# Kernel tuning notes

Measured on AMD Instinct MI355X. Metric: run time of the kernel, lower is better.

## Reference

```python
import jax, jax.numpy as jnp
import numpy as np

B, L, J, D_MODEL, N_HIDDEN = 8, 2048, 2048, 1024, 1024


def setup_inputs() -> dict:
    key = jax.random.key(0)
    ks = jax.random.split(key, 6)
    scale = 1.0 / np.sqrt(D_MODEL)
    return {
        "q": jax.random.normal(ks[0], (B, L, D_MODEL), dtype=jnp.float32),
        "k": jax.random.normal(ks[1], (B, J, D_MODEL), dtype=jnp.float32),
        "v": jax.random.normal(ks[2], (B, J, D_MODEL), dtype=jnp.float32),
        "mask": jnp.zeros((B, L, J), dtype=jnp.float32),
        # Linear(d_model, n_hidden, bias=False) weights, stored [n_hidden, d_model] like torch
        "W_q": jax.random.normal(ks[3], (N_HIDDEN, D_MODEL), dtype=jnp.float32) * scale,
        "W_k": jax.random.normal(ks[4], (N_HIDDEN, D_MODEL), dtype=jnp.float32) * scale,
        "W_v": jax.random.normal(ks[5], (N_HIDDEN, D_MODEL), dtype=jnp.float32) * scale,
    }


def reference(q, k, v, mask, W_q, W_k, W_v):
    # Linear projections (torch Linear: x @ W.T)
    qp = jnp.einsum('bld,hd->blh', q, W_q)
    kp = jnp.einsum('bjd,hd->bjh', k, W_k)
    vp = jnp.einsum('bjd,hd->bjh', v, W_v)
    # scaled dot-product scores [B, L, J]
    scores = jnp.einsum('blh,bjh->blj', qp, kp) / jnp.sqrt(jnp.float32(N_HIDDEN)).astype(qp.dtype)
    scores = scores + mask
    attn = jax.nn.softmax(scores, axis=-1)
    return jnp.einsum('blj,bjh->blh', attn, vp)
```

## Files before the change

kernel.cpp:

```cpp
#include <hip/hip_runtime.h>
#include <hip/hip_fp16.h>

typedef _Float16 f16;
typedef __attribute__((ext_vector_type(8))) _Float16 f16x8;
typedef __attribute__((ext_vector_type(4))) _Float16 f16x4;
typedef __attribute__((ext_vector_type(4))) float f32x4;

#define BM 256
#define BN 256
#define BK 32

__device__ __forceinline__ void gll16(const void* src, void* dst) {
  __builtin_amdgcn_global_load_lds((const __attribute__((address_space(1))) void*)src,
                                   (__attribute__((address_space(3))) void*)dst,
                                   16, 0, 0);
}

template<int MODE>
__global__ __launch_bounds__(512, 2)
void gemm_bt(const f16* __restrict__ Aall, const f16* __restrict__ Ball,
             void* __restrict__ Call,
             int M, int N, int K, int lda, int ldb, int ldc,
             long strideA, long strideB, long strideC,
             const float* __restrict__ maskAll, long strideMask,
             float* __restrict__ lvec, float scale)
{
  __shared__ __align__(16) f16 smA[3][BM * BK];
  __shared__ __align__(16) f16 smB[3][BN * BK];

  unsigned gx = gridDim.x, gy = gridDim.y;
  unsigned id = (blockIdx.z * gy + blockIdx.y) * gx + blockIdx.x;
  unsigned nwg = gx * gy * gridDim.z;
  unsigned swz = (id & 7) * (nwg >> 3) + (id >> 3);
  unsigned bx = swz % gx, rem = swz / gx;
  unsigned by = rem % gy, bz = rem / gy;

  const int z = bz;
  const f16* A = Aall + (long)z * strideA;
  const f16* B = Ball + (long)z * strideB;

  const int tid  = threadIdx.x;
  const int wid  = tid >> 6;
  const int lane = tid & 63;
  const int wm = wid >> 2;
  const int wn = wid & 3;
  const int lr = lane & 15;
  const int g  = lane >> 4;

  const long brow = (long)by * BM;
  const long bcol = (long)bx * BN;
  const int  nt   = K / BK;

  f32x4 acc[8][4] = {};

  auto stA = [&](int buf, int t) {
    #pragma unroll
    for (int i = 0; i < 2; ++i) {
      int c   = i * 512 + tid;
      int row = c >> 2;
      gll16(A + (brow + row) * (long)lda + t * BK + (c & 3) * 8, &smA[buf][c * 8]);
    }
  };
  auto stB = [&](int buf, int t) {
    #pragma unroll
    for (int i = 0; i < 2; ++i) {
      int c   = i * 512 + tid;
      int row = c >> 2;
      gll16(B + (bcol + row) * (long)ldb + t * BK + (c & 3) * 8, &smB[buf][c * 8]);
    }
  };
  auto ld = [&](const f16* base, int r) -> f16x8 {
    return *(const f16x8*)(base + r * BK + g * 8);
  };

  stA(0, 0); stB(0, 0);
  stA(1, 1); stB(1, 1);
  asm volatile("s_waitcnt vmcnt(4)" ::: "memory");
  __builtin_amdgcn_s_barrier();

  int b0 = 0, bn = 2;
  for (int kt = 0; kt < nt; ++kt) {
    const f16* sa = smA[b0];
    const f16* sb = smB[b0];
    const bool pf = (kt + 2 < nt);
    f16x8 af[4], bf[4];

    #pragma unroll
    for (int n = 0; n < 4; ++n) bf[n] = ld(sb, wn * 64 + n * 16 + lr);
    #pragma unroll
    for (int m = 0; m < 4; ++m) af[m] = ld(sa, wm * 128 + m * 16 + lr);
    if (pf) stA(bn, kt + 2);
    __builtin_amdgcn_s_barrier();
    asm volatile("s_waitcnt lgkmcnt(0)" ::: "memory");
    __builtin_amdgcn_sched_barrier(0);
    __builtin_amdgcn_s_setprio(1);
    #pragma unroll
    for (int m = 0; m < 4; ++m)
      #pragma unroll
      for (int n = 0; n < 4; ++n)
        acc[m][n] = __builtin_amdgcn_mfma_f32_16x16x32_f16(af[m], bf[n], acc[m][n], 0, 0, 0);
    __builtin_amdgcn_s_setprio(0);
    __builtin_amdgcn_s_barrier();

    #pragma unroll
    for (int m = 0; m < 4; ++m) af[m] = ld(sa, wm * 128 + 64 + m * 16 + lr);
    if (pf) stB(bn, kt + 2);
    __builtin_amdgcn_s_barrier();
    asm volatile("s_waitcnt lgkmcnt(0)" ::: "memory");
    __builtin_amdgcn_sched_barrier(0);
    __builtin_amdgcn_s_setprio(1);
    #pragma unroll
    for (int m = 0; m < 4; ++m)
      #pragma unroll
      for (int n = 0; n < 4; ++n)
        acc[m + 4][n] = __builtin_amdgcn_mfma_f32_16x16x32_f16(af[m], bf[n], acc[m + 4][n], 0, 0, 0);
    __builtin_amdgcn_s_setprio(0);
    __builtin_amdgcn_sched_barrier(0);
    if (pf) { asm volatile("s_waitcnt vmcnt(4)" ::: "memory"); }
    else    { asm volatile("s_waitcnt vmcnt(0)" ::: "memory"); }
    __builtin_amdgcn_s_barrier();
    b0 = b0 + 1 == 3 ? 0 : b0 + 1;
    bn = bn + 1 == 3 ? 0 : bn + 1;
  }

  const int rb = (lane >> 4) * 4;

  if (MODE == 0) {
    f16* C = (f16*)Call + (long)z * strideC;
    #pragma unroll
    for (int m = 0; m < 8; ++m)
      #pragma unroll
      for (int j = 0; j < 4; ++j) {
        long grow = brow + wm * 128 + m * 16 + rb + j;
        #pragma unroll
        for (int n = 0; n < 4; ++n) {
          long gcol = bcol + wn * 64 + n * 16 + lr;
          C[grow * ldc + gcol] = (f16)acc[m][n][j];
        }
      }
  } else if (MODE == 1) {
    f16* C = (f16*)Call + (long)z * strideC;
    const float* mask = maskAll + (long)z * strideMask;
    #pragma unroll
    for (int m = 0; m < 8; ++m)
      #pragma unroll
      for (int j = 0; j < 4; ++j) {
        long grow = brow + wm * 128 + m * 16 + rb + j;
        float s = 0.f;
        #pragma unroll
        for (int n = 0; n < 4; ++n) {
          long gcol = bcol + wn * 64 + n * 16 + lr;
          float p = __expf(acc[m][n][j] * scale + mask[grow * ldc + gcol]);
          C[grow * ldc + gcol] = (f16)p;
          s += p;
        }
        s += __shfl_xor(s, 1);
        s += __shfl_xor(s, 2);
        s += __shfl_xor(s, 4);
        s += __shfl_xor(s, 8);
        if (lr == 0)
          lvec[((long)z * M + grow) * 32 + bx * 4 + wn] = s;
      }
  } else {
    float* C = (float*)Call + (long)z * strideC;
    #pragma unroll
    for (int m = 0; m < 8; ++m)
      #pragma unroll
      for (int j = 0; j < 4; ++j) {
        long grow = brow + wm * 128 + m * 16 + rb + j;
        float inv = 1.0f / lvec[(long)z * M + grow];
        #pragma unroll
        for (int n = 0; n < 4; ++n) {
          long gcol = bcol + wn * 64 + n * 16 + lr;
          C[grow * ldc + gcol] = acc[m][n][j] * inv;
        }
      }
  }
}

__global__ void cvt_all(const float* __restrict__ q, const float* __restrict__ k,
                        const float* __restrict__ v, const float* __restrict__ Wq,
                        const float* __restrict__ Wk, const float* __restrict__ Wv,
                        f16* __restrict__ qf, f16* __restrict__ kf, f16* __restrict__ vf,
                        f16* __restrict__ Wqf, f16* __restrict__ Wkf, f16* __restrict__ Wvf)
{
  const long NQ4 = 4194304, NW4 = 262144;
  const long total = 3 * NQ4 + 3 * NW4;
  for (long i = (long)blockIdx.x * blockDim.x + threadIdx.x; i < total;
       i += (long)gridDim.x * blockDim.x) {
    const float* src; f16* dst; long j = i;
    if      (j <     NQ4)           { src = q;  dst = qf; }
    else if (j < 2 * NQ4)           { src = k;  dst = kf;  j -= NQ4; }
    else if (j < 3 * NQ4)           { src = v;  dst = vf;  j -= 2 * NQ4; }
    else if (j < 3 * NQ4 + NW4)     { src = Wq; dst = Wqf; j -= 3 * NQ4; }
    else if (j < 3 * NQ4 + 2 * NW4) { src = Wk; dst = Wkf; j -= 3 * NQ4 + NW4; }
    else                            { src = Wv; dst = Wvf; j -= 3 * NQ4 + 2 * NW4; }
    float4 vv = ((const float4*)src)[j];
    f16x4 o;
    o[0] = (f16)vv.x; o[1] = (f16)vv.y; o[2] = (f16)vv.z; o[3] = (f16)vv.w;
    ((f16x4*)dst)[j] = o;
  }
}

__global__ void reduce_l(const float* __restrict__ lpart, float* __restrict__ lsum, int n) {
  int i = blockIdx.x * blockDim.x + threadIdx.x;
  if (i < n) {
    float s = 0.f;
    #pragma unroll
    for (int j = 0; j < 32; ++j) s += lpart[(long)i * 32 + j];
    lsum[i] = s;
  }
}

extern "C" void kernel_launch(void* const* d_in, const int* in_sizes, int n_in,
                              void* d_out, int out_size, void* d_ws, size_t ws_size,
                              hipStream_t stream)
{
  const float* q    = (const float*)d_in[0];
  const float* k    = (const float*)d_in[1];
  const float* v    = (const float*)d_in[2];
  const float* mask = (const float*)d_in[3];
  const float* Wq   = (const float*)d_in[4];
  const float* Wk   = (const float*)d_in[5];
  const float* Wv   = (const float*)d_in[6];
  float* out = (float*)d_out;
  char*  ws  = (char*)d_ws;

  f16* qf  = (f16*)(ws + 0);
  f16* kf  = (f16*)(ws + 33554432);
  f16* vf  = (f16*)(ws + 67108864);
  f16* Pm  = (f16*)(ws + 0);
  f16* Wqf = (f16*)(ws + 100663296);
  f16* Wkf = (f16*)(ws + 102760448);
  f16* Wvf = (f16*)(ws + 104857600);
  f16* qp  = (f16*)(ws + 106954752);
  f16* kp  = (f16*)(ws + 140509184);
  f16* vpT = (f16*)(ws + 174063616);
  float* lpart = (float*)(ws + 207618048);
  float* lsum  = (float*)(ws + 209715200);

  const long L = 2048, J = 2048, D = 1024, H = 1024;

  cvt_all<<<dim3(2048), dim3(256), 0, stream>>>(q, k, v, Wq, Wk, Wv, qf, kf, vf, Wqf, Wkf, Wvf);

  gemm_bt<0><<<dim3(1024 / BN, 16384 / BM, 1), dim3(512), 0, stream>>>(
      qf, Wqf, qp, 16384, 1024, 1024, 1024, 1024, 1024,
      0, 0, 0, nullptr, 0, nullptr, 0.f);
  gemm_bt<0><<<dim3(1024 / BN, 16384 / BM, 1), dim3(512), 0, stream>>>(
      kf, Wkf, kp, 16384, 1024, 1024, 1024, 1024, 1024,
      0, 0, 0, nullptr, 0, nullptr, 0.f);
  gemm_bt<0><<<dim3(2048 / BN, 1024 / BM, 8), dim3(512), 0, stream>>>(
      Wvf, vf, vpT, 1024, 2048, 1024, 1024, 1024, 2048,
      0, J * D, H * J, nullptr, 0, nullptr, 0.f);

  gemm_bt<1><<<dim3(2048 / BN, 2048 / BM, 8), dim3(512), 0, stream>>>(
      qp, kp, Pm, 2048, 2048, 1024, 1024, 1024, 2048,
      L * H, J * H, L * J, mask, L * J, lpart, 0.03125f);

  reduce_l<<<dim3(16384 / 256), dim3(256), 0, stream>>>(lpart, lsum, 16384);

  gemm_bt<2><<<dim3(1024 / BN, 2048 / BM, 8), dim3(512), 0, stream>>>(
      Pm, vpT, out, 2048, 1024, 2048, 2048, 2048, 1024,
      L * J, H * J, L * H, nullptr, 0, lsum, 0.f);
}
```

Before: 385.3 us.

## Deepen GEMM K-tile to 64 with XOR-swizzled LDS and quarter-tile ping-pong pipeline

```diff
diff --git a/kernel.cpp b/kernel.cpp
--- a/kernel.cpp
+++ b/kernel.cpp
@@ -8,7 +8,7 @@
 
 #define BM 256
 #define BN 256
-#define BK 32
+#define BK 64
 
 __device__ __forceinline__ void gll16(const void* src, void* dst) {
   __builtin_amdgcn_global_load_lds((const __attribute__((address_space(1))) void*)src,
@@ -25,8 +25,8 @@
              const float* __restrict__ maskAll, long strideMask,
              float* __restrict__ lvec, float scale)
 {
-  __shared__ __align__(16) f16 smA[3][BM * BK];
-  __shared__ __align__(16) f16 smB[3][BN * BK];
+  __shared__ __align__(16) f16 smA[2][BM * BK];
+  __shared__ __align__(16) f16 smB[2][BN * BK];
 
   unsigned gx = gridDim.x, gy = gridDim.y;
   unsigned id = (blockIdx.z * gy + blockIdx.y) * gx + blockIdx.x;
@@ -52,75 +52,92 @@
   const int  nt   = K / BK;
 
   f32x4 acc[8][4] = {};
-
-  auto stA = [&](int buf, int t) {
+  f16x8 af[8], bf[8];
+
+  auto stage_half = [&](f16* dst, const f16* src, long prow, int ld_, int rowOff, int t) {
     #pragma unroll
     for (int i = 0; i < 2; ++i) {
-      int c   = i * 512 + tid;
-      int row = c >> 2;
-      gll16(A + (brow + row) * (long)lda + t * BK + (c & 3) * 8, &smA[buf][c * 8]);
+      int c  = i * 512 + tid;
+      int r  = c >> 3;
+      int sl = (c & 7) ^ (r & 7);
+      gll16(src + (prow + rowOff + r) * (long)ld_ + t * BK + sl * 8,
+            dst + rowOff * BK + c * 8);
     }
   };
-  auto stB = [&](int buf, int t) {
-    #pragma unroll
-    for (int i = 0; i < 2; ++i) {
-      int c   = i * 512 + tid;
-      int row = c >> 2;
-      gll16(B + (bcol + row) * (long)ldb + t * BK + (c & 3) * 8, &smB[buf][c * 8]);
-    }
-  };
-  auto ld = [&](const f16* base, int r) -> f16x8 {
-    return *(const f16x8*)(base + r * BK + g * 8);
-  };
-
-  stA(0, 0); stB(0, 0);
-  stA(1, 1); stB(1, 1);
-  asm volatile("s_waitcnt vmcnt(4)" ::: "memory");
-  __builtin_amdgcn_s_barrier();
-
-  int b0 = 0, bn = 2;
-  for (int kt = 0; kt < nt; ++kt) {
-    const f16* sa = smA[b0];
-    const f16* sb = smB[b0];
-    const bool pf = (kt + 2 < nt);
-    f16x8 af[4], bf[4];
-
-    #pragma unroll
-    for (int n = 0; n < 4; ++n) bf[n] = ld(sb, wn * 64 + n * 16 + lr);
-    #pragma unroll
-    for (int m = 0; m < 4; ++m) af[m] = ld(sa, wm * 128 + m * 16 + lr);
-    if (pf) stA(bn, kt + 2);
+  auto rdA = [&](const f16* sa, int mh) {
+    #pragma unroll
+    for (int fm = 0; fm < 4; ++fm)
+      #pragma unroll
+      for (int ks = 0; ks < 2; ++ks) {
+        int r = wm * 128 + mh * 64 + fm * 16 + lr;
+        af[fm * 2 + ks] = *(const f16x8*)(sa + r * BK + ((ks * 4 + g) ^ (r & 7)) * 8);
+      }
+  };
+  auto rdB = [&](const f16* sb, int nh) {
+    #pragma unroll
+    for (int fn = 0; fn < 2; ++fn)
+      #pragma unroll
+      for (int ks = 0; ks < 2; ++ks) {
+        int r = wn * 64 + (nh * 2 + fn) * 16 + lr;
+        bf[(nh * 2 + fn) * 2 + ks] = *(const f16x8*)(sb + r * BK + ((ks * 4 + g) ^ (r & 7)) * 8);
+      }
+  };
+  auto sync_mfma = [&](int fm0, int fn0) {
     __builtin_amdgcn_s_barrier();
     asm volatile("s_waitcnt lgkmcnt(0)" ::: "memory");
     __builtin_amdgcn_sched_barrier(0);
     __builtin_amdgcn_s_setprio(1);
     #pragma unroll
-    for (int m = 0; m < 4; ++m)
-      #pragma unroll
-      for (int n = 0; n < 4; ++n)
-        acc[m][n] = __builtin_amdgcn_mfma_f32_16x16x32_f16(af[m], bf[n], acc[m][n], 0, 0, 0);
+    for (int fm = 0; fm < 4; ++fm)
+      #pragma unroll
+      for (int fn = 0; fn < 2; ++fn)
+        #pragma unroll
+        for (int ks = 0; ks < 2; ++ks)
+          acc[fm0 + fm][fn0 + fn] = __builtin_amdgcn_mfma_f32_16x16x32_f16(
+              af[fm * 2 + ks], bf[(fn0 + fn) * 2 + ks], acc[fm0 + fm][fn0 + fn], 0, 0, 0);
     __builtin_amdgcn_s_setprio(0);
     __builtin_amdgcn_s_barrier();
-
-    #pragma unroll
-    for (int m = 0; m < 4; ++m) af[m] = ld(sa, wm * 128 + 64 + m * 16 + lr);
-    if (pf) stB(bn, kt + 2);
-    __builtin_amdgcn_s_barrier();
-    asm volatile("s_waitcnt lgkmcnt(0)" ::: "memory");
-    __builtin_amdgcn_sched_barrier(0);
-    __builtin_amdgcn_s_setprio(1);
-    #pragma unroll
-    for (int m = 0; m < 4; ++m)
-      #pragma unroll
-      for (int n = 0; n < 4; ++n)
-        acc[m + 4][n] = __builtin_amdgcn_mfma_f32_16x16x32_f16(af[m], bf[n], acc[m + 4][n], 0, 0, 0);
-    __builtin_amdgcn_s_setprio(0);
-    __builtin_amdgcn_sched_barrier(0);
-    if (pf) { asm volatile("s_waitcnt vmcnt(4)" ::: "memory"); }
-    else    { asm volatile("s_waitcnt vmcnt(0)" ::: "memory"); }
-    __builtin_amdgcn_s_barrier();
-    b0 = b0 + 1 == 3 ? 0 : b0 + 1;
-    bn = bn + 1 == 3 ? 0 : bn + 1;
+  };
+
+  stage_half(smA[0], A, brow, lda, 0, 0);
+  stage_half(smA[0], A, brow, lda, 128, 0);
+  stage_half(smB[0], B, bcol, ldb, 0, 0);
+  stage_half(smB[0], B, bcol, ldb, 128, 0);
+  stage_half(smB[1], B, bcol, ldb, 0, 1);
+  stage_half(smB[1], B, bcol, ldb, 128, 1);
+  asm volatile("s_waitcnt vmcnt(4)" ::: "memory");
+  __builtin_amdgcn_s_barrier();
+
+  const int niter = nt / 2;
+  for (int i = 0; i < niter; ++i) {
+    const bool last = (i == niter - 1);
+    const int t2 = 2 * i + 2, t3 = 2 * i + 3;
+
+    rdA(smA[0], 0); rdB(smB[0], 0);
+    stage_half(smA[1], A, brow, lda, 0, 2 * i + 1);
+    sync_mfma(0, 0);
+    rdB(smB[0], 1);
+    stage_half(smA[1], A, brow, lda, 128, 2 * i + 1);
+    sync_mfma(0, 2);
+    rdA(smA[0], 1);
+    if (t2 < nt) stage_half(smB[0], B, bcol, ldb, 0, t2);
+    sync_mfma(4, 2);
+    if (t2 < nt) stage_half(smB[0], B, bcol, ldb, 128, t2);
+    if (!last) { asm volatile("s_waitcnt vmcnt(4)" ::: "memory"); }
+    else       { asm volatile("s_waitcnt vmcnt(0)" ::: "memory"); }
+    sync_mfma(4, 0);
+    rdA(smA[1], 0); rdB(smB[1], 0);
+    if (t2 < nt) stage_half(smA[0], A, brow, lda, 0, t2);
+    sync_mfma(0, 0);
+    rdB(smB[1], 1);
+    if (t2 < nt) stage_half(smA[0], A, brow, lda, 128, t2);
+    sync_mfma(0, 2);
+    rdA(smA[1], 1);
+    if (t3 < nt) stage_half(smB[1], B, bcol, ldb, 0, t3);
+    sync_mfma(4, 2);
+    if (t3 < nt) stage_half(smB[1], B, bcol, ldb, 128, t3);
+    if (!last) { asm volatile("s_waitcnt vmcnt(4)" ::: "memory"); }
+    sync_mfma(4, 0);
   }
 
   const int rb = (lane >> 4) * 4;
```

After: 377.0 us. -2.1%, faster.
